# Kernel optimization log

Measured on AMD Instinct MI355X. Metric: run time of the kernel, lower is better.

Reference implementation:

```python
import jax, jax.numpy as jnp
import numpy as np

B, S, V, E, R1, R2, L = 16, 128, 32000, 128, 256, 640, 512


def pos_encoding(seq_len, d, n=10000.0):
    # P[k, 2i] = sin(k / n^(2i/d)); P[k, 2i+1] = cos(k / n^(2i/d))
    k = jnp.arange(seq_len, dtype=jnp.float32)[:, None]
    i = jnp.arange(d // 2, dtype=jnp.float32)[None, :]
    ang = k / jnp.power(jnp.float32(n), 2.0 * i / d)
    P = jnp.zeros((seq_len, d), dtype=jnp.float32)
    P = P.at[:, 0::2].set(jnp.sin(ang)).at[:, 1::2].set(jnp.cos(ang))
    return P


def setup_inputs() -> dict:
    key = jax.random.key(0)
    ks = iter(jax.random.split(key, 40))

    def lin(fin, fout):
        W = jax.random.normal(next(ks), (fin, fout), jnp.float32) / np.sqrt(fin)
        b = jax.random.normal(next(ks), (fout,), jnp.float32) * 0.01
        return W, b

    inp = {}
    inp['x'] = jax.random.normal(next(ks), (B, S, V), jnp.float32)
    inp['W_emb'], inp['b_emb'] = lin(V, E)
    inp['W_pos1'], inp['b_pos1'] = lin(2 * E, E)
    inp['W_red'], inp['b_red'] = lin(S * E, R1)
    inp['W_pos2'], inp['b_pos2'] = lin(2 * R1, R1)
    inp['W_red2'], inp['b_red2'] = lin(S * R1, R2)
    inp['W_pos3'], inp['b_pos3'] = lin(2 * R2, R2)
    inp['W_down2'], inp['b_down2'] = lin(R2, L)
    inp['W_flat'], inp['b_flat'] = lin(L * S, L)
    inp['W_d1'], inp['b_d1'] = lin(L, L)
    inp['W_d2'], inp['b_d2'] = lin(L, L)
    inp['W_d3'], inp['b_d3'] = lin(L, L)
    inp['W_p1'], inp['b_p1'] = lin(L, V)
    inp['W_p2'], inp['b_p2'] = lin(L, V)
    return inp


def _square_memory(h):
    # einsum('bij,bkm->bikj') factorizes: out[b,i,k,j] = h[b,i,j] * sum_m h[b,k,m]
    b, s, d = h.shape
    row_sum = h.sum(axis=-1)                       # (B, S)
    q = h[:, :, None, :] * row_sum[:, None, :, None]  # (B, S, S, D)
    return q.reshape(b, s, s * d)


def reference(x, W_emb, b_emb, W_pos1, b_pos1, W_red, b_red, W_pos2, b_pos2,
              W_red2, b_red2, W_pos3, b_pos3, W_down2, b_down2, W_flat, b_flat,
              W_d1, b_d1, W_d2, b_d2, W_d3, b_d3, W_p1, b_p1, W_p2, b_p2):
    relu = jax.nn.relu
    h = relu(x @ W_emb + b_emb)                                  # (B,S,E)
    h = h + relu(pos_encoding(S, 2 * E) @ W_pos1 + b_pos1)
    h = relu(_square_memory(h) @ W_red + b_red)                  # (B,S,R1)
    h = h + relu(pos_encoding(S, 2 * R1) @ W_pos2 + b_pos2)
    h = relu(_square_memory(h) @ W_red2 + b_red2)                # (B,S,R2)
    h = h + relu(pos_encoding(S, 2 * R2) @ W_pos3 + b_pos3)
    h = relu(h @ W_down2 + b_down2)                              # (B,S,L)
    h = relu(h.reshape(h.shape[0], -1) @ W_flat + b_flat)        # (B,L)
    h = relu(h @ W_d1 + b_d1)
    p1 = h @ W_p1 + b_p1
    h = relu(h @ W_d2 + b_d2)
    p2 = h @ W_p2 + b_p2
    h = relu(h @ W_d3 + b_d3)
    p3 = h @ W_p1 + b_p1  # faithful to source: project_1 reused (project_3 unused)
    return p1 + p2 + p3
```

## Files before the change

### kernel.cpp

```cpp
#include <hip/hip_runtime.h>

typedef float  f4   __attribute__((ext_vector_type(4)));
typedef __bf16 bf8_t __attribute__((ext_vector_type(8)));
typedef __bf16 bf4_t __attribute__((ext_vector_type(4)));

__device__ __forceinline__ void glds16(const void* g, void* l) {
    __builtin_amdgcn_global_load_lds(
        (const __attribute__((address_space(1))) void*)g,
        (__attribute__((address_space(3))) void*)l, 16, 0, 0);
}

__global__ __launch_bounds__(256)
void prep_kernel(float* __restrict__ P1, float* __restrict__ P2,
                 float* __restrict__ P3,
                 const float* __restrict__ bp1, const float* __restrict__ bp2,
                 float* __restrict__ bc, float* __restrict__ rs2,
                 const float* __restrict__ Wemb, __bf16* __restrict__ WembT,
                 const float* __restrict__ Wd2, __bf16* __restrict__ Wd2T,
                 const float* __restrict__ Wq1, __bf16* __restrict__ Wq1T,
                 const float* __restrict__ Wq2, __bf16* __restrict__ Wq2T,
                 const float* __restrict__ Wq3, __bf16* __restrict__ Wq3T) {
    const int bid = blockIdx.x;
    const int t = threadIdx.x;
    if (bid < 5280) {
        const float* src; __bf16* dst; int CN, RK, tn, local;
        if (bid < 4000)      { src = Wemb; dst = WembT; RK = 32000; CN = 128; tn = 4;  local = bid; }
        else if (bid < 4320) { src = Wd2;  dst = Wd2T;  RK = 640;   CN = 512; tn = 16; local = bid - 4000; }
        else if (bid < 4352) { src = Wq1;  dst = Wq1T;  RK = 256;   CN = 128; tn = 4;  local = bid - 4320; }
        else if (bid < 4480) { src = Wq2;  dst = Wq2T;  RK = 512;   CN = 256; tn = 8;  local = bid - 4352; }
        else                 { src = Wq3;  dst = Wq3T;  RK = 1280;  CN = 640; tn = 20; local = bid - 4480; }
        const int kt = local / tn, ntl = local - kt * tn;
        const int k0 = kt * 32, n0 = ntl * 32;
        __shared__ float tile[32][33];
        const int r = t >> 3, c4 = (t & 7) * 4;
        const f4 v = *(const f4*)(src + (long)(k0 + r) * CN + n0 + c4);
        tile[r][c4] = v[0]; tile[r][c4 + 1] = v[1];
        tile[r][c4 + 2] = v[2]; tile[r][c4 + 3] = v[3];
        __syncthreads();
        bf4_t o2;
        o2[0] = (__bf16)tile[c4][r];     o2[1] = (__bf16)tile[c4 + 1][r];
        o2[2] = (__bf16)tile[c4 + 2][r]; o2[3] = (__bf16)tile[c4 + 3][r];
        *(bf4_t*)(dst + (long)(n0 + r) * RK + k0 + c4) = o2;
        return;
    }
    int idx = (bid - 5280) * 256 + t;
    const int n1 = 128 * 256, n2 = 128 * 512;
    const int nP = 262144;
    if (idx < nP) {
        float* P; int d, local;
        if (idx < n1)           { P = P1; d = 256;  local = idx; }
        else if (idx < n1 + n2) { P = P2; d = 512;  local = idx - n1; }
        else                    { P = P3; d = 1280; local = idx - n1 - n2; }
        int s = local / d;
        int k = local - s * d;
        int i = k >> 1;
        float ang = (float)s * powf(10000.0f, (-2.0f * (float)i) / (float)d);
        P[local] = (k & 1) ? cosf(ang) : sinf(ang);
    } else if (idx < nP + 32000) {
        int j = idx - nP;
        bc[j] = 2.f * bp1[j] + bp2[j];
    } else if (idx < nP + 32000 + 2048) {
        rs2[idx - nP - 32000] = 0.f;
    }
}

template<int BMODE>
__device__ __forceinline__ void gemm_dev(
    float* As0, float* As1, float* Bb0, float* Bb1,
    const float* __restrict__ A, const void* __restrict__ Bv,
    const void* __restrict__ B2v, float* __restrict__ C,
    const float* __restrict__ bias, const float* __restrict__ addsrc,
    float* __restrict__ rsum,
    int M, int N, int K, int lda, int ldb, int ldc, int kswitch,
    long sA, long sB, long sC, int ksplit, int kchunk, int relu,
    int bn, int bm, int bz) {

    const int t = threadIdx.x;
    const int batch = bz / ksplit;
    const int kz = bz - batch * ksplit;
    const int m0 = bm * 64, n0 = bn * 128;
    const int kb = kz * kchunk;
    const int ke = (kb + kchunk < K) ? (kb + kchunk) : K;
    const int nit = (ke - kb + 31) >> 5;

    const int lane = t & 63;
    const int w = t >> 6;
    const int wm = w >> 1, wn = w & 1;
    const int fr = lane & 15;
    const int fq = (lane >> 4) * 8;

    f4 acc[2][4];
#pragma unroll
    for (int mt = 0; mt < 2; ++mt)
#pragma unroll
        for (int nt = 0; nt < 4; ++nt) acc[mt][nt] = (f4){0.f, 0.f, 0.f, 0.f};

    const float* Ab = A + (long)batch * sA;
    const int mvalid = M - m0;

    const int ra = t >> 3;
    const int ja = (t & 7) ^ (ra & 7);
    const float* aS0 = Ab + (long)(m0 + ra) * lda + 4 * ja;
    const float* aS1 = aS0 + 32L * lda;

    const __bf16* bTS0 = nullptr; const __bf16* bTS1 = nullptr;
    const float* bNS0 = nullptr; const float* bNS2 = nullptr;
    if constexpr (BMODE == 0) {
        const __bf16* BT = (const __bf16*)Bv + (long)batch * sB;
        const int nb = t >> 2;
        const int fb = (nb & 3) ^ ((nb >> 2) & 3);
        const int jb = (t & 3) ^ fb;
        bTS0 = BT + (long)(n0 + nb) * ldb + 8 * jb;
        bTS1 = bTS0 + 64L * ldb;
    } else {
        const float* Bn = (const float*)Bv + (long)batch * sB;
        bNS0 = Bn + (long)(t >> 5) * ldb + n0 + (t & 31) * 4;
        const float* Bn2 = (const float*)(B2v ? B2v : Bv);
        bNS2 = Bn2 + (long)(t >> 5) * ldb + n0 + (t & 31) * 4;
    }

    auto STAGE = [&](float* Ad, float* Bd, int k0) {
        if (ra < mvalid)      glds16(aS0 + k0, Ad + 4 * t);
        if (ra + 32 < mvalid) glds16(aS1 + k0, Ad + 1024 + 4 * t);
        if constexpr (BMODE == 0) {
            glds16(bTS0 + k0, Bd + 4 * t);
            glds16(bTS1 + k0, Bd + 1024 + 4 * t);
        } else {
            const float* bp = (k0 < kswitch) ? (bNS0 + (long)k0 * ldb)
                                             : (bNS2 + (long)(k0 - kswitch) * ldb);
            glds16(bp,             Bd + 4 * t);
            glds16(bp + 8L * ldb,  Bd + 1024 + 4 * t);
            glds16(bp + 16L * ldb, Bd + 2048 + 4 * t);
            glds16(bp + 24L * ldb, Bd + 3072 + 4 * t);
        }
    };

    const int R0 = wm * 32 + fr, R1 = R0 + 16;
    const int jq = (lane >> 4) * 2;
    const int x7 = R0 & 7;
    const int aO00 = R0 * 8 + (jq ^ x7);
    const int aO01 = R0 * 8 + ((jq + 1) ^ x7);
    const int aO10 = R1 * 8 + (jq ^ x7);
    const int aO11 = R1 * 8 + ((jq + 1) ^ x7);
    int bOf[4];
    if constexpr (BMODE == 0) {
        const int fbc = (fr & 3) ^ ((fr >> 2) & 3);
        const int jb2 = (lane >> 4) ^ fbc;
#pragma unroll
        for (int nt = 0; nt < 4; ++nt)
            bOf[nt] = ((wn * 64 + nt * 16 + fr) * 4 + jb2) * 8;
    } else {
#pragma unroll
        for (int nt = 0; nt < 4; ++nt)
            bOf[nt] = wn * 64 + nt * 16 + fr;
    }

    STAGE(As0, Bb0, kb);
    __syncthreads();
    int cur = 0;
    for (int i = 0; i < nit; ++i) {
        float* Ac = cur ? As1 : As0;
        float* Bc = cur ? Bb1 : Bb0;
        if (i + 1 < nit) STAGE(cur ? As0 : As1, cur ? Bb0 : Bb1, kb + (i + 1) * 32);

        f4 x0 = *(const f4*)(Ac + aO00 * 4);
        f4 x1 = *(const f4*)(Ac + aO01 * 4);
        f4 x2 = *(const f4*)(Ac + aO10 * 4);
        f4 x3 = *(const f4*)(Ac + aO11 * 4);
        bf8_t af0, af1;
#pragma unroll
        for (int q = 0; q < 4; ++q) {
            af0[q] = (__bf16)x0[q]; af0[4 + q] = (__bf16)x1[q];
            af1[q] = (__bf16)x2[q]; af1[4 + q] = (__bf16)x3[q];
        }
#pragma unroll
        for (int nt = 0; nt < 4; ++nt) {
            bf8_t bv;
            if constexpr (BMODE == 0) {
                bv = *(const bf8_t*)((const __bf16*)Bc + bOf[nt]);
            } else {
                const float* bb = Bc + fq * 128 + bOf[nt];
#pragma unroll
                for (int d = 0; d < 8; ++d) bv[d] = (__bf16)bb[d * 128];
            }
            acc[0][nt] = __builtin_amdgcn_mfma_f32_16x16x32_bf16(af0, bv, acc[0][nt], 0, 0, 0);
            acc[1][nt] = __builtin_amdgcn_mfma_f32_16x16x32_bf16(af1, bv, acc[1][nt], 0, 0, 0);
        }
        __syncthreads();
        cur ^= 1;
    }

    float* Cp; long ldcp;
    const bool fin = (ksplit == 1);
    if (!fin) { Cp = C + (long)(batch * ksplit + kz) * M * N; ldcp = N; }
    else      { Cp = C + (long)batch * sC;                    ldcp = ldc; }

    const int rb = m0 + wm * 32 + (lane >> 4) * 4;
    const int cb_ = n0 + wn * 64 + fr;
    float rowpart[2][4] = {{0.f,0.f,0.f,0.f},{0.f,0.f,0.f,0.f}};
#pragma unroll
    for (int mt = 0; mt < 2; ++mt) {
#pragma unroll
        for (int nt = 0; nt < 4; ++nt) {
            const int c = cb_ + nt * 16;
            const float bvl = (fin && bias) ? bias[c] : 0.f;
#pragma unroll
            for (int v = 0; v < 4; ++v) {
                const int r = rb + mt * 16 + v;
                if (r < M) {
                    float val = acc[mt][nt][v] + bvl;
                    if (fin && relu) val = fmaxf(val, 0.f);
                    if (fin && addsrc) val += addsrc[(long)r * ldcp + c];
                    Cp[(long)r * ldcp + c] = val;
                    rowpart[mt][v] += val;
                }
            }
        }
    }
    if (rsum) {
#pragma unroll
        for (int mt = 0; mt < 2; ++mt) {
#pragma unroll
            for (int v = 0; v < 4; ++v) {
                float s = rowpart[mt][v];
                s += __shfl_xor(s, 1); s += __shfl_xor(s, 2);
                s += __shfl_xor(s, 4); s += __shfl_xor(s, 8);
                const int r = rb + mt * 16 + v;
                if (fr == 0 && r < M) atomicAdd(&rsum[(long)bz * M + r], s);
            }
        }
    }
}

template<int BMODE>
__global__ __launch_bounds__(256)
void gemm_v2(const float* A, const void* Bv, const void* B2v, float* C,
             const float* bias, const float* addsrc, float* rsum,
             int M, int N, int K, int lda, int ldb, int ldc, int kswitch,
             long sA, long sB, long sC, int ksplit, int kchunk, int relu) {
    __shared__ __align__(16) float AsF[2][2048];
    __shared__ __align__(16) float Bbuf[2][BMODE ? 4096 : 2048];
    gemm_dev<BMODE>(&AsF[0][0], &AsF[1][0], &Bbuf[0][0], &Bbuf[1][0],
                    A, Bv, B2v, C, bias, addsrc, rsum,
                    M, N, K, lda, ldb, ldc, kswitch, sA, sB, sC,
                    ksplit, kchunk, relu,
                    blockIdx.x, blockIdx.y, blockIdx.z);
}

__global__ __launch_bounds__(256)
void mega1_kernel(const float* __restrict__ x, const __bf16* __restrict__ WembT,
                  float* __restrict__ partG1,
                  const float* __restrict__ P1, const __bf16* __restrict__ Q1T,
                  float* __restrict__ Q1o, const float* __restrict__ bq1,
                  const float* __restrict__ P2, const __bf16* __restrict__ Q2T,
                  float* __restrict__ Q2o, const float* __restrict__ bq2,
                  const float* __restrict__ P3, const __bf16* __restrict__ Q3T,
                  float* __restrict__ Q3o, const float* __restrict__ bq3) {
    __shared__ __align__(16) float AsF[2][2048];
    __shared__ __align__(16) float Bbuf[2][2048];
    float* A0 = &AsF[0][0]; float* A1 = &AsF[1][0];
    float* B0 = &Bbuf[0][0]; float* B1 = &Bbuf[1][0];
    const int bid = blockIdx.x;
    if (bid < 1024) {
        const int xc = bid & 7, j = bid >> 3;
        const int bz = xc + ((j >> 5) << 3);
        const int bm = j & 31;
        gemm_dev<0>(A0, A1, B0, B1, x, WembT, nullptr, partG1,
                    nullptr, nullptr, nullptr,
                    2048, 128, 32000, 32000, 32000, 128, 32000,
                    0, 0, 0, 32, 1024, 0, 0, bm, bz);
    } else if (bid < 1026) {
        gemm_dev<0>(A0, A1, B0, B1, P1, Q1T, nullptr, Q1o,
                    bq1, nullptr, nullptr,
                    128, 128, 256, 256, 256, 128, 256,
                    0, 0, 0, 1, 256, 1, 0, bid - 1024, 0);
    } else if (bid < 1030) {
        const int l = bid - 1026;
        gemm_dev<0>(A0, A1, B0, B1, P2, Q2T, nullptr, Q2o,
                    bq2, nullptr, nullptr,
                    128, 256, 512, 512, 512, 256, 512,
                    0, 0, 0, 1, 512, 1, l & 1, l >> 1, 0);
    } else {
        const int l = bid - 1030;
        gemm_dev<0>(A0, A1, B0, B1, P3, Q3T, nullptr, Q3o,
                    bq3, nullptr, nullptr,
                    128, 640, 1280, 1280, 1280, 640, 1280,
                    0, 0, 0, 1, 1280, 1, l % 5, l / 5, 0);
    }
}

__global__ __launch_bounds__(256)
void reduce_splitk(const float* __restrict__ part, float* __restrict__ outp,
                   const float* __restrict__ bias, int MN, int N, int ksplit,
                   int relu) {
    int idx = blockIdx.x * 256 + threadIdx.x;
    if (idx >= MN) return;
    float s = 0.f;
    for (int z = 0; z < ksplit; ++z) s += part[(long)z * MN + idx];
    if (bias) s += bias[idx % N];
    if (relu) s = fmaxf(s, 0.f);
    outp[idx] = s;
}

__global__ __launch_bounds__(256)
void reduce_rs_kernel(const float* __restrict__ part, float* __restrict__ h1,
                      const float* __restrict__ bias, const float* __restrict__ Q1,
                      float* __restrict__ rs1, int ksplit) {
    const int t = threadIdx.x;
    const int idx = blockIdx.x * 256 + t;
    float s = 0.f;
    for (int z = 0; z < ksplit; ++z) s += part[(long)z * 262144 + idx];
    s += bias[idx & 127];
    s = fmaxf(s, 0.f);
    s += Q1[idx & 16383];
    h1[idx] = s;
    float r = s;
    for (int off = 32; off > 0; off >>= 1) r += __shfl_down(r, off, 64);
    __shared__ float p[4];
    const int w = t >> 6, lane = t & 63;
    if (lane == 0) p[w] = r;
    __syncthreads();
    if (t < 2) rs1[(blockIdx.x << 1) + t] = p[t * 2] + p[t * 2 + 1];
}

extern "C" void kernel_launch(void* const* d_in, const int* in_sizes, int n_in,
                              void* d_out, int out_size, void* d_ws, size_t ws_size,
                              hipStream_t stream) {
    const float* x       = (const float*)d_in[0];
    const float* W_emb   = (const float*)d_in[1];
    const float* b_emb   = (const float*)d_in[2];
    const float* W_pos1  = (const float*)d_in[3];
    const float* b_pos1  = (const float*)d_in[4];
    const float* W_red   = (const float*)d_in[5];
    const float* b_red   = (const float*)d_in[6];
    const float* W_pos2  = (const float*)d_in[7];
    const float* b_pos2  = (const float*)d_in[8];
    const float* W_red2  = (const float*)d_in[9];
    const float* b_red2  = (const float*)d_in[10];
    const float* W_pos3  = (const float*)d_in[11];
    const float* b_pos3  = (const float*)d_in[12];
    const float* W_down2 = (const float*)d_in[13];
    const float* b_down2 = (const float*)d_in[14];
    const float* W_flat  = (const float*)d_in[15];
    const float* b_flat  = (const float*)d_in[16];
    const float* W_d1    = (const float*)d_in[17];
    const float* b_d1    = (const float*)d_in[18];
    const float* W_d2    = (const float*)d_in[19];
    const float* b_d2    = (const float*)d_in[20];
    const float* W_d3    = (const float*)d_in[21];
    const float* b_d3    = (const float*)d_in[22];
    const float* W_p1    = (const float*)d_in[23];
    const float* b_p1    = (const float*)d_in[24];
    const float* W_p2    = (const float*)d_in[25];
    const float* b_p2    = (const float*)d_in[26];
    float* out = (float*)d_out;
    float* ws  = (float*)d_ws;

    size_t o = 0;
    auto alloc = [&](size_t n) { size_t p = o; o += (n + 63) & ~(size_t)63; return p; };
    const size_t oP1 = alloc(128 * 256);
    const size_t oP2 = alloc(128 * 512);
    const size_t oP3 = alloc(128 * 1280);
    const size_t oQ1 = alloc(128 * 128);
    const size_t oQ2 = alloc(128 * 256);
    const size_t oQ3 = alloc(128 * 640);
    const size_t oBC = alloc(32000);
    const size_t oH1 = alloc(2048 * 128);
    const size_t oRS1 = alloc(2048);
    const size_t oRS2 = alloc(2048);
    const size_t oH2 = alloc(2048 * 256);
    const size_t oH3 = alloc(2048 * 640);
    const size_t oH4 = alloc(2048 * 512);
    const size_t oH5 = alloc(16 * 512);
    const size_t oH6c = alloc(16 * 1024);
    const size_t oCat = alloc(16 * 1024);
    const size_t oM1 = alloc(16 * 32768);
    const size_t oM2 = alloc(16 * 163840);
    const size_t oWembT = alloc(2048000);
    const size_t oWd2T  = alloc(163840);
    const size_t oQ1T   = alloc(16384);
    const size_t oQ2T   = alloc(65536);
    const size_t oQ3T   = alloc(409600);
    const size_t oRegA = alloc(32u * 262144);
    const size_t oPartG1 = oRegA, oPartF = oRegA;
    (void)ws_size; (void)in_sizes; (void)n_in; (void)out_size;

    __bf16* WembT = (__bf16*)(ws + oWembT);
    __bf16* Wd2T  = (__bf16*)(ws + oWd2T);
    __bf16* Q1T   = (__bf16*)(ws + oQ1T);
    __bf16* Q2T   = (__bf16*)(ws + oQ2T);
    __bf16* Q3T   = (__bf16*)(ws + oQ3T);

    dim3 blk(256);

    prep_kernel<<<dim3(6437), blk, 0, stream>>>(
        ws + oP1, ws + oP2, ws + oP3, b_p1, b_p2, ws + oBC, ws + oRS2,
        W_emb, WembT, W_down2, Wd2T, W_pos1, Q1T, W_pos2, Q2T, W_pos3, Q3T);
    mega1_kernel<<<dim3(1040), blk, 0, stream>>>(
        x, WembT, ws + oPartG1,
        ws + oP1, Q1T, ws + oQ1, b_pos1,
        ws + oP2, Q2T, ws + oQ2, b_pos2,
        ws + oP3, Q3T, ws + oQ3, b_pos3);
    reduce_rs_kernel<<<dim3(1024), blk, 0, stream>>>(ws + oPartG1, ws + oH1,
                                                     b_emb, ws + oQ1, ws + oRS1, 32);
    gemm_v2<1><<<dim3(256, 1, 1), blk, 0, stream>>>(ws + oRS1, W_red, nullptr,
        ws + oM1, nullptr, nullptr, nullptr,
        16, 32768, 128, 128, 32768, 32768, 128, 0, 0, 0, 1, 128, 0);
    gemm_v2<1><<<dim3(2, 2, 16), blk, 0, stream>>>(ws + oH1, ws + oM1, nullptr,
        ws + oH2, b_red, ws + oQ2, ws + oRS2,
        128, 256, 128, 128, 256, 256, 128, 16384, 32768, 32768, 1, 128, 1);
    gemm_v2<1><<<dim3(1280, 1, 1), blk, 0, stream>>>(ws + oRS2, W_red2, nullptr,
        ws + oM2, nullptr, nullptr, nullptr,
        16, 163840, 128, 128, 163840, 163840, 128, 0, 0, 0, 1, 128, 0);
    gemm_v2<1><<<dim3(5, 2, 16), blk, 0, stream>>>(ws + oH2, ws + oM2, nullptr,
        ws + oH3, b_red2, ws + oQ3, nullptr,
        128, 640, 256, 256, 640, 640, 256, 32768, 163840, 81920, 1, 256, 1);
    gemm_v2<0><<<dim3(4, 32, 1), blk, 0, stream>>>(ws + oH3, Wd2T, nullptr,
        ws + oH4, b_down2, nullptr, nullptr,
        2048, 512, 640, 640, 640, 512, 640, 0, 0, 0, 1, 640, 1);
    gemm_v2<1><<<dim3(4, 1, 64), blk, 0, stream>>>(ws + oH4, W_flat, nullptr,
        ws + oPartF, nullptr, nullptr, nullptr,
        16, 512, 65536, 65536, 512, 512, 65536, 0, 0, 0, 64, 1024, 0);
    reduce_splitk<<<dim3(32), blk, 0, stream>>>(ws + oPartF, ws + oH5, b_flat,
                                                8192, 512, 64, 1);
    gemm_v2<1><<<dim3(4, 1, 1), blk, 0, stream>>>(ws + oH5, W_d1, nullptr,
        ws + oH6c, b_d1, nullptr, nullptr,
        16, 512, 512, 512, 512, 1024, 512, 0, 0, 0, 1, 512, 1);
    gemm_v2<1><<<dim3(4, 1, 1), blk, 0, stream>>>(ws + oH6c, W_d2, nullptr,
        ws + oCat + 512, b_d2, nullptr, nullptr,
        16, 512, 512, 1024, 512, 1024, 512, 0, 0, 0, 1, 512, 1);
    gemm_v2<1><<<dim3(4, 1, 1), blk, 0, stream>>>(ws + oCat + 512, W_d3, nullptr,
        ws + oCat, b_d3, ws + oH6c, nullptr,
        16, 512, 512, 1024, 512, 1024, 512, 0, 0, 0, 1, 512, 1);
    gemm_v2<1><<<dim3(250, 1, 1), blk, 0, stream>>>(ws + oCat, W_p1, W_p2,
        out, ws + oBC, nullptr, nullptr,
        16, 32000, 1024, 1024, 32000, 32000, 512, 0, 0, 0, 1, 1024, 0);
}
```

Baseline: 363.1 us.

## Replace LDS-staged embedding GEMM with register-direct MFMA loads and 40-way split-K

The large x@W_emb GEMM no longer stages tiles through shared memory. A new register-only path loads fp32 x and bf16 WembT straight from global memory into MFMA operands, fully unrolled over an 800-wide K chunk. The split-K factor goes from 32 to 40, which gives more blocks, and the reduce kernel and workspace are resized to match. Other GEMM launches get kswitch set to 1<<30, which looks like it disables a B2 switch that was not needed. The trade is the loss of LDS reuse and of coalesced staging, in exchange for fewer barriers and more parallelism.

```diff
diff --git a/kernel.cpp b/kernel.cpp
--- a/kernel.cpp
+++ b/kernel.cpp
@@ -159,8 +159,8 @@
     __syncthreads();
     int cur = 0;
     for (int i = 0; i < nit; ++i) {
-        float* Ac = cur ? As1 : As0;
-        float* Bc = cur ? Bb1 : Bb0;
+        const float* Ac = cur ? As1 : As0;
+        const float* Bc = cur ? Bb1 : Bb0;
         if (i + 1 < nit) STAGE(cur ? As0 : As1, cur ? Bb0 : Bb1, kb + (i + 1) * 32);
 
         f4 x0 = *(const f4*)(Ac + aO00 * 4);
@@ -181,7 +181,7 @@
             } else {
                 const float* bb = Bc + fq * 128 + bOf[nt];
 #pragma unroll
-                for (int d = 0; d < 8; ++d) bv[d] = (__bf16)bb[d * 128];
+                for (int d2 = 0; d2 < 8; ++d2) bv[d2] = (__bf16)bb[d2 * 128];
             }
             acc[0][nt] = __builtin_amdgcn_mfma_f32_16x16x32_bf16(af0, bv, acc[0][nt], 0, 0, 0);
             acc[1][nt] = __builtin_amdgcn_mfma_f32_16x16x32_bf16(af1, bv, acc[1][nt], 0, 0, 0);
@@ -230,6 +230,70 @@
             }
         }
     }
+}
+
+__device__ __forceinline__ void gemm1_reg(const float* __restrict__ x,
+                                          const __bf16* __restrict__ WembT,
+                                          float* __restrict__ part,
+                                          int bm, int kz) {
+    const int t = threadIdx.x;
+    const int lane = t & 63, w = t >> 6;
+    const int wm = w >> 1, wn = w & 1;
+    const int fr = lane & 15;
+    const int fq = (lane >> 4) * 8;
+    const int m0 = bm * 64;
+    const int kb = kz * 800;
+
+    const float* aB0 = x + (long)(m0 + wm * 32 + fr) * 32000 + kb + fq;
+    const float* aB1 = aB0 + 16L * 32000;
+    const __bf16* bB0 = WembT + (long)(wn * 64 +  0 + fr) * 32000 + kb + fq;
+    const __bf16* bB1 = WembT + (long)(wn * 64 + 16 + fr) * 32000 + kb + fq;
+    const __bf16* bB2 = WembT + (long)(wn * 64 + 32 + fr) * 32000 + kb + fq;
+    const __bf16* bB3 = WembT + (long)(wn * 64 + 48 + fr) * 32000 + kb + fq;
+
+    f4 acc[2][4];
+#pragma unroll
+    for (int mt = 0; mt < 2; ++mt)
+#pragma unroll
+        for (int nt = 0; nt < 4; ++nt) acc[mt][nt] = (f4){0.f, 0.f, 0.f, 0.f};
+
+#pragma unroll
+    for (int i = 0; i < 25; ++i) {
+        const int k = i * 32;
+        f4 a0 = *(const f4*)(aB0 + k);
+        f4 a1 = *(const f4*)(aB0 + k + 4);
+        f4 a2 = *(const f4*)(aB1 + k);
+        f4 a3 = *(const f4*)(aB1 + k + 4);
+        bf8_t b0 = *(const bf8_t*)(bB0 + k);
+        bf8_t b1 = *(const bf8_t*)(bB1 + k);
+        bf8_t b2 = *(const bf8_t*)(bB2 + k);
+        bf8_t b3 = *(const bf8_t*)(bB3 + k);
+        bf8_t af0, af1;
+#pragma unroll
+        for (int q = 0; q < 4; ++q) {
+            af0[q] = (__bf16)a0[q]; af0[4 + q] = (__bf16)a1[q];
+            af1[q] = (__bf16)a2[q]; af1[4 + q] = (__bf16)a3[q];
+        }
+        acc[0][0] = __builtin_amdgcn_mfma_f32_16x16x32_bf16(af0, b0, acc[0][0], 0, 0, 0);
+        acc[1][0] = __builtin_amdgcn_mfma_f32_16x16x32_bf16(af1, b0, acc[1][0], 0, 0, 0);
+        acc[0][1] = __builtin_amdgcn_mfma_f32_16x16x32_bf16(af0, b1, acc[0][1], 0, 0, 0);
+        acc[1][1] = __builtin_amdgcn_mfma_f32_16x16x32_bf16(af1, b1, acc[1][1], 0, 0, 0);
+        acc[0][2] = __builtin_amdgcn_mfma_f32_16x16x32_bf16(af0, b2, acc[0][2], 0, 0, 0);
+        acc[1][2] = __builtin_amdgcn_mfma_f32_16x16x32_bf16(af1, b2, acc[1][2], 0, 0, 0);
+        acc[0][3] = __builtin_amdgcn_mfma_f32_16x16x32_bf16(af0, b3, acc[0][3], 0, 0, 0);
+        acc[1][3] = __builtin_amdgcn_mfma_f32_16x16x32_bf16(af1, b3, acc[1][3], 0, 0, 0);
+    }
+
+    float* Cp = part + (long)kz * 262144;
+    const int rb = m0 + wm * 32 + (lane >> 4) * 4;
+    const int cb_ = wn * 64 + fr;
+#pragma unroll
+    for (int mt = 0; mt < 2; ++mt)
+#pragma unroll
+        for (int nt = 0; nt < 4; ++nt)
+#pragma unroll
+            for (int v = 0; v < 4; ++v)
+                Cp[(long)(rb + mt * 16 + v) * 128 + cb_ + nt * 16] = acc[mt][nt][v];
 }
 
 template<int BMODE>
@@ -261,27 +325,24 @@
     float* A0 = &AsF[0][0]; float* A1 = &AsF[1][0];
     float* B0 = &Bbuf[0][0]; float* B1 = &Bbuf[1][0];
     const int bid = blockIdx.x;
-    if (bid < 1024) {
+    if (bid < 1280) {
         const int xc = bid & 7, j = bid >> 3;
-        const int bz = xc + ((j >> 5) << 3);
+        const int kz = xc + ((j >> 5) << 3);
         const int bm = j & 31;
-        gemm_dev<0>(A0, A1, B0, B1, x, WembT, nullptr, partG1,
-                    nullptr, nullptr, nullptr,
-                    2048, 128, 32000, 32000, 32000, 128, 32000,
-                    0, 0, 0, 32, 1024, 0, 0, bm, bz);
-    } else if (bid < 1026) {
+        gemm1_reg(x, WembT, partG1, bm, kz);
+    } else if (bid < 1282) {
         gemm_dev<0>(A0, A1, B0, B1, P1, Q1T, nullptr, Q1o,
                     bq1, nullptr, nullptr,
                     128, 128, 256, 256, 256, 128, 256,
-                    0, 0, 0, 1, 256, 1, 0, bid - 1024, 0);
-    } else if (bid < 1030) {
-        const int l = bid - 1026;
+                    0, 0, 0, 1, 256, 1, 0, bid - 1280, 0);
+    } else if (bid < 1286) {
+        const int l = bid - 1282;
         gemm_dev<0>(A0, A1, B0, B1, P2, Q2T, nullptr, Q2o,
                     bq2, nullptr, nullptr,
                     128, 256, 512, 512, 512, 256, 512,
                     0, 0, 0, 1, 512, 1, l & 1, l >> 1, 0);
     } else {
-        const int l = bid - 1030;
+        const int l = bid - 1286;
         gemm_dev<0>(A0, A1, B0, B1, P3, Q3T, nullptr, Q3o,
                     bq3, nullptr, nullptr,
                     128, 640, 1280, 1280, 1280, 640, 1280,
@@ -381,7 +442,7 @@
     const size_t oQ1T   = alloc(16384);
     const size_t oQ2T   = alloc(65536);
     const size_t oQ3T   = alloc(409600);
-    const size_t oRegA = alloc(32u * 262144);
+    const size_t oRegA = alloc(40u * 262144);
     const size_t oPartG1 = oRegA, oPartF = oRegA;
     (void)ws_size; (void)in_sizes; (void)n_in; (void)out_size;
 
@@ -396,42 +457,42 @@
     prep_kernel<<<dim3(6437), blk, 0, stream>>>(
         ws + oP1, ws + oP2, ws + oP3, b_p1, b_p2, ws + oBC, ws + oRS2,
         W_emb, WembT, W_down2, Wd2T, W_pos1, Q1T, W_pos2, Q2T, W_pos3, Q3T);
-    mega1_kernel<<<dim3(1040), blk, 0, stream>>>(
+    mega1_kernel<<<dim3(1296), blk, 0, stream>>>(
         x, WembT, ws + oPartG1,
         ws + oP1, Q1T, ws + oQ1, b_pos1,
         ws + oP2, Q2T, ws + oQ2, b_pos2,
         ws + oP3, Q3T, ws + oQ3, b_pos3);
     reduce_rs_kernel<<<dim3(1024), blk, 0, stream>>>(ws + oPartG1, ws + oH1,
-                                                     b_emb, ws + oQ1, ws + oRS1, 32);
+                                                     b_emb, ws + oQ1, ws + oRS1, 40);
     gemm_v2<1><<<dim3(256, 1, 1), blk, 0, stream>>>(ws + oRS1, W_red, nullptr,
         ws + oM1, nullptr, nullptr, nullptr,
-        16, 32768, 128, 128, 32768, 32768, 128, 0, 0, 0, 1, 128, 0);
+        16, 32768, 128, 128, 32768, 32768, 1 << 30, 0, 0, 0, 1, 128, 0);
     gemm_v2<1><<<dim3(2, 2, 16), blk, 0, stream>>>(ws + oH1, ws + oM1, nullptr,
         ws + oH2, b_red, ws + oQ2, ws + oRS2,
-        128, 256, 128, 128, 256, 256, 128, 16384, 32768, 32768, 1, 128, 1);
+        128, 256, 128, 128, 256, 256, 1 << 30, 16384, 32768, 32768, 1, 128, 1);
     gemm_v2<1><<<dim3(1280, 1, 1), blk, 0, stream>>>(ws + oRS2, W_red2, nullptr,
         ws + oM2, nullptr, nullptr, nullptr,
-        16, 163840, 128, 128, 163840, 163840, 128, 0, 0, 0, 1, 128, 0);
+        16, 163840, 128, 128, 163840, 163840, 1 << 30, 0, 0, 0, 1, 128, 0);
     gemm_v2<1><<<dim3(5, 2, 16), blk, 0, stream>>>(ws + oH2, ws + oM2, nullptr,
         ws + oH3, b_red2, ws + oQ3, nullptr,
-        128, 640, 256, 256, 640, 640, 256, 32768, 163840, 81920, 1, 256, 1);
+        128, 640, 256, 256, 640, 640, 1 << 30, 32768, 163840, 81920, 1, 256, 1);
     gemm_v2<0><<<dim3(4, 32, 1), blk, 0, stream>>>(ws + oH3, Wd2T, nullptr,
         ws + oH4, b_down2, nullptr, nullptr,
-        2048, 512, 640, 640, 640, 512, 640, 0, 0, 0, 1, 640, 1);
+        2048, 512, 640, 640, 640, 512, 1 << 30, 0, 0, 0, 1, 640, 1);
     gemm_v2<1><<<dim3(4, 1, 64), blk, 0, stream>>>(ws + oH4, W_flat, nullptr,
         ws + oPartF, nullptr, nullptr, nullptr,
-        16, 512, 65536, 65536, 512, 512, 65536, 0, 0, 0, 64, 1024, 0);
+        16, 512, 65536, 65536, 512, 512, 1 << 30, 0, 0, 0, 64, 1024, 0);
     reduce_splitk<<<dim3(32), blk, 0, stream>>>(ws + oPartF, ws + oH5, b_flat,
                                                 8192, 512, 64, 1);
     gemm_v2<1><<<dim3(4, 1, 1), blk, 0, stream>>>(ws + oH5, W_d1, nullptr,
         ws + oH6c, b_d1, nullptr, nullptr,
-        16, 512, 512, 512, 512, 1024, 512, 0, 0, 0, 1, 512, 1);
+        16, 512, 512, 512, 512, 1024, 1 << 30, 0, 0, 0, 1, 512, 1);
     gemm_v2<1><<<dim3(4, 1, 1), blk, 0, stream>>>(ws + oH6c, W_d2, nullptr,
         ws + oCat + 512, b_d2, nullptr, nullptr,
-        16, 512, 512, 1024, 512, 1024, 512, 0, 0, 0, 1, 512, 1);
+        16, 512, 512, 1024, 512, 1024, 1 << 30, 0, 0, 0, 1, 512, 1);
     gemm_v2<1><<<dim3(4, 1, 1), blk, 0, stream>>>(ws + oCat + 512, W_d3, nullptr,
         ws + oCat, b_d3, ws + oH6c, nullptr,
-        16, 512, 512, 1024, 512, 1024, 512, 0, 0, 0, 1, 512, 1);
+        16, 512, 512, 1024, 512, 1024, 1 << 30, 0, 0, 0, 1, 512, 1);
     gemm_v2<1><<<dim3(250, 1, 1), blk, 0, stream>>>(ws + oCat, W_p1, W_p2,
         out, ws + oBC, nullptr, nullptr,
         16, 32000, 1024, 1024, 32000, 32000, 512, 0, 0, 0, 1, 1024, 0);
```

Measured after the change: 425.4 us. 17.1% more time.
